# Optimization experiments

Measured on AMD Instinct MI355X. Metric: run time of the kernel, lower is better.

The kernel has to match this reference:

```python
import jax, jax.numpy as jnp
import numpy as np

EMBED_DIM = 128
NUM_EDGES = 4096   # edges per graph (power of 2)
BATCH = 64
N_LEAVES = BATCH * NUM_EDGES
NUM_LEVELS = int(np.log2(NUM_EDGES))  # 12


def setup_inputs() -> dict:
    key = jax.random.key(0)
    ks = jax.random.split(key, 4)
    d = EMBED_DIM
    scale = 1.0 / np.sqrt(2 * d)
    return {
        "h_bot": jax.random.normal(ks[0], (N_LEAVES, d), dtype=jnp.float32),
        "c_bot": jax.random.normal(ks[1], (N_LEAVES, d), dtype=jnp.float32),
        "U_iou": jax.random.normal(ks[2], (2 * d, 3 * d), dtype=jnp.float32) * scale,
        "b_iou": jnp.zeros((3 * d,), dtype=jnp.float32),
        "Uf_W": jax.random.normal(ks[3], (2 * d, 2 * d), dtype=jnp.float32) * scale,
        "Uf_b": jnp.zeros((2 * d,), dtype=jnp.float32),
    }


def _cell(hl, cl, hr, cr, U_iou, b_iou, Uf_W, Uf_b):
    # BinaryTreeLSTMCell: combine two child (h, c) states.
    h_cat = jnp.concatenate([hl, hr], axis=-1)          # [n, 2d]
    iou = h_cat @ U_iou + b_iou                          # [n, 3d]
    i, o, u = jnp.split(iou, 3, axis=-1)
    i = jax.nn.sigmoid(i)
    o = jax.nn.sigmoid(o)
    u = jnp.tanh(u)
    f = jax.nn.sigmoid(h_cat @ Uf_W + Uf_b)              # [n, 2d]
    f1, f2 = jnp.split(f, 2, axis=-1)
    c = i * u + f1 * cl + f2 * cr
    h = o * jnp.tanh(c)
    return h, c


def reference(h_bot, c_bot, U_iou, b_iou, Uf_W, Uf_b):
    # Per-level Fenwick merge: left children are states[0::2], right are
    # states[1::2] (as in get_list_indices), combined by the tree-LSTM cell.
    h, c = h_bot, c_bot
    for _ in range(NUM_LEVELS):
        h, c = _cell(h[0::2], c[0::2], h[1::2], c[1::2],
                     U_iou, b_iou, Uf_W, Uf_b)
    # one (h, c) root state per graph -> [BATCH, 2*EMBED_DIM]
    return jnp.concatenate([h, c], axis=-1)
```

## Files before the change

kernel.cpp:

```cpp
#include <hip/hip_runtime.h>
#include <hip/hip_bf16.h>
#include <stdint.h>


#define DEV __device__ __forceinline__

typedef __attribute__((ext_vector_type(8))) short bf16x8;
typedef __attribute__((ext_vector_type(4))) float f32x4;

DEV float bf2f(unsigned short u) {
    union { uint32_t i; float f; } v; v.i = ((uint32_t)u) << 16; return v.f;
}
DEV unsigned short f2bf(float f) {
    union { float f; uint32_t i; } v; v.f = f;
    uint32_t u = v.i;
    return (unsigned short)((u + 0x7FFFu + ((u >> 16) & 1u)) >> 16);
}
DEV unsigned short truncbf(float f) {
    union { float f; uint32_t i; } v; v.f = f; return (unsigned short)(v.i >> 16);
}
DEV float sigm(float x) { return 1.0f / (1.0f + __expf(-x)); }
DEV float tanh_(float x) {
    x = fminf(fmaxf(x, -15.f), 15.f);
    float e = __expf(2.0f * x);
    return (e - 1.0f) / (e + 1.0f);
}
DEV float ldmix(const void* p, size_t i, int bf) {
    return bf ? bf2f(((const unsigned short*)p)[i]) : ((const float*)p)[i];
}

__global__ void pack_w(const void* __restrict__ h_bot,
                       const void* __restrict__ U_iou, const void* __restrict__ Uf_W,
                       const void* __restrict__ b_iou, const void* __restrict__ uf_b,
                       int* __restrict__ flag_out, float* __restrict__ bias_out,
                       unsigned short* __restrict__ Wp) {
    __shared__ int total;
    const int tid = threadIdx.x;
    if (tid == 0) total = 0;
    __syncthreads();
    const unsigned short* hs = (const unsigned short*)h_bot;
    int local = 0;
    #pragma unroll
    for (int i = 0; i < 4; ++i) {
        unsigned short s = hs[tid * 4 + i];
        int e = (s >> 7) & 0xFF;
        local += (e >= 100 && e <= 134) ? 1 : 0;
    }
    atomicAdd(&total, local);
    __syncthreads();
    const int flag = (total > 820) ? 1 : 0;

    if (blockIdx.x == 0) {
        if (tid == 0) *flag_out = flag;
        for (int i = tid; i < 384; i += 256) bias_out[i]       = ldmix(b_iou, i, flag);
        for (int i = tid; i < 256; i += 256) bias_out[384 + i] = ldmix(uf_b, i, flag);
    }

    int idx  = blockIdx.x * 256 + tid;
    int j    = idx / 20480;
    int rem  = idx % 20480;
    int g    = rem / 4096;
    int rem2 = rem & 4095;
    int ks   = rem2 >> 9;
    int lane = (rem2 >> 3) & 63;
    int jj   = rem2 & 7;
    int k = ks * 32 + (lane >> 4) * 8 + jj;
    int t = j * 16 + (lane & 15);
    float w = (g < 3) ? ldmix(U_iou, (size_t)k * 384 + g * 128 + t, flag)
                      : ldmix(Uf_W,  (size_t)k * 256 + (g - 3) * 128 + t, flag);
    unsigned short hi = truncbf(w);
    unsigned short lo = f2bf(w - bf2f(hi));
    size_t base = (size_t)j * 40960;
    int fb = (g * 8 + ks) * 512 + lane * 8 + jj;
    Wp[base + fb]         = hi;
    Wp[base + 20480 + fb] = lo;
}

template<int IN_MODE, bool LEAN, bool FINAL, bool JSPLIT, int BLK, int MT>
__global__ __launch_bounds__(BLK, (BLK == 512 ? 4 : 2))
void level_kernel(const void* __restrict__ h_in,
                  const unsigned short* __restrict__ h_lo_in,
                  const void* __restrict__ c_in_v,
                  const unsigned short* __restrict__ Wp,
                  const int* __restrict__ flag_p,
                  const float* __restrict__ bias,
                  unsigned short* __restrict__ h_hi_out,
                  unsigned short* __restrict__ h_lo_out,
                  void* __restrict__ c_out_v,
                  void* __restrict__ final_out,
                  int M_out) {
    __shared__ __align__(16) unsigned short ldsW[40960];
    const int tid  = threadIdx.x;
    const int lane = tid & 63;
    const int w    = tid >> 6;
    const int ROWS = (BLK / 64) * MT * 16;
    const int R0   = blockIdx.x * ROWS + w * MT * 16;
    const int mrow = lane & 15;
    const int quad = lane >> 4;
    const int flag = (IN_MODE == 0 || FINAL) ? *flag_p : 0;

    const int    M_in   = 2 * M_out;
    const size_t PS_in  = (size_t)M_in  * 16;
    const size_t PS_out = (size_t)M_out * 16;

    bf16x8 a_hi[MT][8], a_lo[MT][8];
    #pragma unroll
    for (int mt = 0; mt < MT; ++mt) {
        int r = R0 + mt * 16 + mrow;
        if (r >= M_out) r = M_out - 1;
        #pragma unroll
        for (int ks = 0; ks < 8; ++ks) {
            if (IN_MODE == 0) {
                size_t base = ((size_t)(2 * r + (ks >> 2))) * 128 + (ks & 3) * 32 + quad * 8;
                if (flag) {
                    a_hi[mt][ks] = *(const bf16x8*)((const unsigned short*)h_in + base);
                    bf16x8 z;
                    #pragma unroll
                    for (int e = 0; e < 8; ++e) z[e] = 0;
                    a_lo[mt][ks] = z;
                } else {
                    const float* hf = (const float*)h_in;
                    f32x4 x0 = *(const f32x4*)(hf + base);
                    f32x4 x1 = *(const f32x4*)(hf + base + 4);
                    bf16x8 hv, lv;
                    #pragma unroll
                    for (int e = 0; e < 4; ++e) {
                        float x = x0[e];
                        unsigned short hh = truncbf(x);
                        hv[e] = (short)hh; lv[e] = (short)f2bf(x - bf2f(hh));
                    }
                    #pragma unroll
                    for (int e = 0; e < 4; ++e) {
                        float x = x1[e];
                        unsigned short hh = truncbf(x);
                        hv[4 + e] = (short)hh; lv[4 + e] = (short)f2bf(x - bf2f(hh));
                    }
                    a_hi[mt][ks] = hv; a_lo[mt][ks] = lv;
                }
            } else {
                int jpl = (ks & 3) * 2 + (quad >> 1);
                size_t base = (size_t)jpl * PS_in
                            + (size_t)(2 * r + (ks >> 2)) * 16 + (quad & 1) * 8;
                a_hi[mt][ks] = *(const bf16x8*)((const unsigned short*)h_in + base);
                if (IN_MODE == 1)
                    a_lo[mt][ks] = *(const bf16x8*)(h_lo_in + base);
            }
        }
    }

    const bf16x8* ldsV = (const bf16x8*)ldsW;
    const int jN = JSPLIT ? 1 : 8;

    #pragma unroll 1
    for (int jj = 0; jj < jN; ++jj) {
        const int j = JSPLIT ? (int)blockIdx.y : ((jj + (int)blockIdx.x) & 7);
        __syncthreads();
        {
            const bf16x8* src = (const bf16x8*)(Wp + (size_t)j * 40960);
            bf16x8*       dst = (bf16x8*)ldsW;
            #pragma unroll
            for (int it = tid; it < 5120; it += BLK)
                dst[it] = src[it];
        }
        __syncthreads();

        f32x4 acc[5][MT];
        #pragma unroll
        for (int g = 0; g < 5; ++g)
            #pragma unroll
            for (int mt = 0; mt < MT; ++mt)
                acc[g][mt] = f32x4{0.f, 0.f, 0.f, 0.f};
        #pragma unroll
        for (int ks = 0; ks < 8; ++ks) {
            #pragma unroll
            for (int g = 0; g < 5; ++g) {
                bf16x8 bhi = ldsV[(g * 8 + ks) * 64 + lane];
                bf16x8 blo = ldsV[(40 + g * 8 + ks) * 64 + lane];
                #pragma unroll
                for (int mt = 0; mt < MT; ++mt) {
                    acc[g][mt] = __builtin_amdgcn_mfma_f32_16x16x32_bf16(a_hi[mt][ks], bhi, acc[g][mt], 0, 0, 0);
                    if (IN_MODE != 2)
                        acc[g][mt] = __builtin_amdgcn_mfma_f32_16x16x32_bf16(a_lo[mt][ks], bhi, acc[g][mt], 0, 0, 0);
                    acc[g][mt] = __builtin_amdgcn_mfma_f32_16x16x32_bf16(a_hi[mt][ks], blo, acc[g][mt], 0, 0, 0);
                }
            }
        }

        const int t = j * 16 + mrow;
        const float bi   = bias[t];
        const float bo   = bias[128 + t];
        const float bu   = bias[256 + t];
        const float bf1v = bias[384 + t];
        const float bf2v = bias[512 + t];
        #pragma unroll
        for (int mt = 0; mt < MT; ++mt) {
            #pragma unroll
            for (int p = 0; p < 4; ++p) {
                int r = R0 + mt * 16 + quad * 4 + p;
                if (r < M_out) {
                    float iv = sigm(acc[0][mt][p] + bi);
                    float ov = sigm(acc[1][mt][p] + bo);
                    float uv = tanh_(acc[2][mt][p] + bu);
                    float f1 = sigm(acc[3][mt][p] + bf1v);
                    float f2 = sigm(acc[4][mt][p] + bf2v);
                    float cl, cr;
                    if (IN_MODE == 0) {
                        size_t li = ((size_t)(2 * r)) * 128 + t;
                        cl = ldmix(c_in_v, li, flag);
                        cr = ldmix(c_in_v, li + 128, flag);
                    } else {
                        size_t cb = (size_t)j * PS_in + (size_t)(2 * r) * 16 + mrow;
                        if (IN_MODE == 1) {
                            cl = ((const float*)c_in_v)[cb];
                            cr = ((const float*)c_in_v)[cb + 16];
                        } else {
                            cl = bf2f(((const unsigned short*)c_in_v)[cb]);
                            cr = bf2f(((const unsigned short*)c_in_v)[cb + 16]);
                        }
                    }
                    float c = fmaf(iv, uv, fmaf(f1, cl, f2 * cr));
                    float h = ov * tanh_(c);
                    if (FINAL) {
                        if (flag) {
                            unsigned short* o = (unsigned short*)final_out;
                            o[(size_t)r * 256 + t]       = f2bf(h);
                            o[(size_t)r * 256 + 128 + t] = f2bf(c);
                        } else {
                            float* o = (float*)final_out;
                            o[(size_t)r * 256 + t]       = h;
                            o[(size_t)r * 256 + 128 + t] = c;
                        }
                    } else {
                        size_t so = (size_t)j * PS_out + (size_t)r * 16 + mrow;
                        if (LEAN) {
                            h_hi_out[so] = f2bf(h);
                            ((unsigned short*)c_out_v)[so] = f2bf(c);
                        } else {
                            unsigned short hh = truncbf(h);
                            h_hi_out[so] = hh;
                            h_lo_out[so] = f2bf(h - bf2f(hh));
                            ((float*)c_out_v)[so] = c;
                        }
                    }
                }
            }
        }
    }
}

extern "C" void kernel_launch(void* const* d_in, const int* in_sizes, int n_in,
                              void* d_out, int out_size, void* d_ws, size_t ws_size,
                              hipStream_t stream) {
    const void* h_bot = d_in[0];
    const void* c_bot = d_in[1];
    const void* U_iou = d_in[2];
    const void* b_iou = d_in[3];
    const void* Uf_W  = d_in[4];
    const void* Uf_b  = d_in[5];
    (void)in_sizes; (void)n_in; (void)out_size;

    const int M0 = 131072;

    char* ws = (char*)d_ws;
    size_t off = 0;
    auto alloc = [&](size_t bytes) -> void* {
        off = (off + 255) & ~(size_t)255;
        void* p = ws + off;
        off += bytes;
        return p;
    };

    int*            flag = (int*)alloc(4);
    float*          bias = (float*)alloc(640 * 4);
    unsigned short* Wp   = (unsigned short*)alloc((size_t)327680 * 2);

    size_t full_need = off + 4096
                     + 2 * (size_t)33554432 + 2 * (size_t)16777216
                     + (size_t)67108864 + (size_t)33554432;
    bool full = (ws_size >= full_need);

    pack_w<<<dim3(640), dim3(256), 0, stream>>>(h_bot, U_iou, Uf_W, b_iou, Uf_b,
                                                flag, bias, Wp);

    if (full) {
        unsigned short* hAhi = (unsigned short*)alloc(33554432);
        unsigned short* hAlo = (unsigned short*)alloc(33554432);
        unsigned short* hBhi = (unsigned short*)alloc(16777216);
        unsigned short* hBlo = (unsigned short*)alloc(16777216);
        float*          cA   = (float*)alloc(67108864);
        float*          cB   = (float*)alloc(33554432);

        level_kernel<0, false, false, false, 512, 1><<<dim3(1024), dim3(512), 0, stream>>>(
            h_bot, nullptr, c_bot, Wp, flag, bias, hAhi, hAlo, cA, nullptr, M0);
        level_kernel<1, false, false, false, 512, 1><<<dim3(512), dim3(512), 0, stream>>>(
            hAhi, hAlo, cA, Wp, flag, bias, hBhi, hBlo, cB, nullptr, M0 >> 1);
        level_kernel<1, false, false, false, 512, 1><<<dim3(256), dim3(512), 0, stream>>>(
            hBhi, hBlo, cB, Wp, flag, bias, hAhi, hAlo, cA, nullptr, M0 >> 2);

        const unsigned short* hi_in = hAhi;
        const unsigned short* lo_in = hAlo;
        const void*           c_in  = cA;
        for (int l = 3; l < 11; ++l) {
            int M = M0 >> l;
            unsigned short* ohi = (l & 1) ? hBhi : hAhi;
            unsigned short* olo = (l & 1) ? hBlo : hAlo;
            float*          oc  = (l & 1) ? cB : cA;
            level_kernel<1, false, false, true, 256, 2>
                <<<dim3((M + 127) / 128, 8), dim3(256), 0, stream>>>(
                hi_in, lo_in, c_in, Wp, flag, bias, ohi, olo, oc, nullptr, M);
            hi_in = ohi; lo_in = olo; c_in = oc;
        }
        level_kernel<1, false, true, true, 256, 2><<<dim3(1, 8), dim3(256), 0, stream>>>(
            hi_in, lo_in, c_in, Wp, flag, bias, nullptr, nullptr, nullptr, d_out, 64);
    } else {
        unsigned short* hA = (unsigned short*)alloc(33554432);
        unsigned short* hB = (unsigned short*)alloc(16777216);
        unsigned short* cA = (unsigned short*)alloc(33554432);
        unsigned short* cB = (unsigned short*)alloc(16777216);

        level_kernel<0, true, false, false, 512, 1><<<dim3(1024), dim3(512), 0, stream>>>(
            h_bot, nullptr, c_bot, Wp, flag, bias, hA, nullptr, cA, nullptr, M0);
        level_kernel<2, true, false, false, 512, 1><<<dim3(512), dim3(512), 0, stream>>>(
            hA, nullptr, cA, Wp, flag, bias, hB, nullptr, cB, nullptr, M0 >> 1);
        level_kernel<2, true, false, false, 512, 1><<<dim3(256), dim3(512), 0, stream>>>(
            hB, nullptr, cB, Wp, flag, bias, hA, nullptr, cA, nullptr, M0 >> 2);

        const unsigned short* h_in = hA;
        const void*           c_in = cA;
        for (int l = 3; l < 11; ++l) {
            int M = M0 >> l;
            unsigned short* oh = (l & 1) ? hB : hA;
            unsigned short* oc = (l & 1) ? cB : cA;
            level_kernel<2, true, false, true, 256, 2>
                <<<dim3((M + 127) / 128, 8), dim3(256), 0, stream>>>(
                h_in, nullptr, c_in, Wp, flag, bias, oh, nullptr, oc, nullptr, M);
            h_in = oh; c_in = oc;
        }
        level_kernel<2, true, true, true, 256, 2><<<dim3(1, 8), dim3(256), 0, stream>>>(
            h_in, nullptr, c_in, Wp, flag, bias, nullptr, nullptr, nullptr, d_out, 64);
    }
}
```

Before: 700.4 us.

## Double-buffer weight staging via async global-to-LDS loads split into hi/lo phases

Splits each output-column tile's weights into two half-size phases (hi and lo terms) and double-buffers them in LDS, loading the next phase with global_load_lds while the current phase's MFMAs run. The c-state loads are moved ahead of the MFMA phase, and MFMA sections run at raised wave priority. This is meant to hide weight staging latency and the per-tile barrier stalls. The cost is more barriers per tile, extra registers for the prefetched c values, and a dependence on how the async LDS load is ordered against the barriers.

```diff
diff --git a/kernel.cpp b/kernel.cpp
--- a/kernel.cpp
+++ b/kernel.cpp
@@ -7,6 +7,9 @@
 
 typedef __attribute__((ext_vector_type(8))) short bf16x8;
 typedef __attribute__((ext_vector_type(4))) float f32x4;
+
+typedef __attribute__((address_space(3))) uint32_t lds_u32_t;
+typedef const __attribute__((address_space(1))) uint32_t glb_u32_t;
 
 DEV float bf2f(unsigned short u) {
     union { uint32_t i; float f; } v; v.i = ((uint32_t)u) << 16; return v.f;
@@ -27,6 +30,17 @@
 }
 DEV float ldmix(const void* p, size_t i, int bf) {
     return bf ? bf2f(((const unsigned short*)p)[i]) : ((const float*)p)[i];
+}
+
+template<int BLK>
+DEV void stage_term(unsigned short* dst, const unsigned short* src, int tid) {
+    constexpr int NIT = 40960 / (BLK * 16);
+    #pragma unroll
+    for (int it = 0; it < NIT; ++it) {
+        int o = (it * BLK + tid) * 8;
+        __builtin_amdgcn_global_load_lds((glb_u32_t*)(src + o),
+                                         (lds_u32_t*)(dst + o), 16, 0, 0);
+    }
 }
 
 __global__ void pack_w(const void* __restrict__ h_bot,
@@ -89,7 +103,7 @@
                   void* __restrict__ c_out_v,
                   void* __restrict__ final_out,
                   int M_out) {
-    __shared__ __align__(16) unsigned short ldsW[40960];
+    __shared__ __align__(16) unsigned short ldsW[2][20480];
     const int tid  = threadIdx.x;
     const int lane = tid & 63;
     const int w    = tid >> 6;
@@ -102,6 +116,15 @@
     const int    M_in   = 2 * M_out;
     const size_t PS_in  = (size_t)M_in  * 16;
     const size_t PS_out = (size_t)M_out * 16;
+
+    const int phN  = JSPLIT ? 2 : 16;
+    const int rot  = JSPLIT ? 0 : (int)blockIdx.x;
+    auto phSrc = [&](int ph) -> const unsigned short* {
+        int j = JSPLIT ? (int)blockIdx.y : ((ph >> 1) + rot) & 7;
+        return Wp + (size_t)j * 40960 + (size_t)(ph & 1) * 20480;
+    };
+
+    stage_term<BLK>(ldsW[0], phSrc(0), tid);
 
     bf16x8 a_hi[MT][8], a_lo[MT][8];
     #pragma unroll
@@ -148,64 +171,35 @@
         }
     }
 
-    const bf16x8* ldsV = (const bf16x8*)ldsW;
-    const int jN = JSPLIT ? 1 : 8;
-
+    __syncthreads();
+
+    f32x4 acc[5][MT];
+    #pragma unroll
+    for (int g = 0; g < 5; ++g)
+        #pragma unroll
+        for (int mt = 0; mt < MT; ++mt)
+            acc[g][mt] = f32x4{0.f, 0.f, 0.f, 0.f};
+    float cpre[MT][4][2];
+
+    int cur = 0;
     #pragma unroll 1
-    for (int jj = 0; jj < jN; ++jj) {
-        const int j = JSPLIT ? (int)blockIdx.y : ((jj + (int)blockIdx.x) & 7);
-        __syncthreads();
-        {
-            const bf16x8* src = (const bf16x8*)(Wp + (size_t)j * 40960);
-            bf16x8*       dst = (bf16x8*)ldsW;
+    for (int ph = 0; ph < phN; ++ph) {
+        const int j    = JSPLIT ? (int)blockIdx.y : ((ph >> 1) + rot) & 7;
+        const int term = ph & 1;
+
+        if (ph + 1 < phN)
+            stage_term<BLK>(ldsW[cur ^ 1], phSrc(ph + 1), tid);
+
+        if (term == 0) {
             #pragma unroll
-            for (int it = tid; it < 5120; it += BLK)
-                dst[it] = src[it];
-        }
-        __syncthreads();
-
-        f32x4 acc[5][MT];
-        #pragma unroll
-        for (int g = 0; g < 5; ++g)
-            #pragma unroll
-            for (int mt = 0; mt < MT; ++mt)
-                acc[g][mt] = f32x4{0.f, 0.f, 0.f, 0.f};
-        #pragma unroll
-        for (int ks = 0; ks < 8; ++ks) {
-            #pragma unroll
-            for (int g = 0; g < 5; ++g) {
-                bf16x8 bhi = ldsV[(g * 8 + ks) * 64 + lane];
-                bf16x8 blo = ldsV[(40 + g * 8 + ks) * 64 + lane];
+            for (int mt = 0; mt < MT; ++mt) {
                 #pragma unroll
-                for (int mt = 0; mt < MT; ++mt) {
-                    acc[g][mt] = __builtin_amdgcn_mfma_f32_16x16x32_bf16(a_hi[mt][ks], bhi, acc[g][mt], 0, 0, 0);
-                    if (IN_MODE != 2)
-                        acc[g][mt] = __builtin_amdgcn_mfma_f32_16x16x32_bf16(a_lo[mt][ks], bhi, acc[g][mt], 0, 0, 0);
-                    acc[g][mt] = __builtin_amdgcn_mfma_f32_16x16x32_bf16(a_hi[mt][ks], blo, acc[g][mt], 0, 0, 0);
-                }
-            }
-        }
-
-        const int t = j * 16 + mrow;
-        const float bi   = bias[t];
-        const float bo   = bias[128 + t];
-        const float bu   = bias[256 + t];
-        const float bf1v = bias[384 + t];
-        const float bf2v = bias[512 + t];
-        #pragma unroll
-        for (int mt = 0; mt < MT; ++mt) {
-            #pragma unroll
-            for (int p = 0; p < 4; ++p) {
-                int r = R0 + mt * 16 + quad * 4 + p;
-                if (r < M_out) {
-                    float iv = sigm(acc[0][mt][p] + bi);
-                    float ov = sigm(acc[1][mt][p] + bo);
-                    float uv = tanh_(acc[2][mt][p] + bu);
-                    float f1 = sigm(acc[3][mt][p] + bf1v);
-                    float f2 = sigm(acc[4][mt][p] + bf2v);
+                for (int p = 0; p < 4; ++p) {
+                    int r = R0 + mt * 16 + quad * 4 + p;
+                    if (r >= M_out) r = M_out - 1;
                     float cl, cr;
                     if (IN_MODE == 0) {
-                        size_t li = ((size_t)(2 * r)) * 128 + t;
+                        size_t li = ((size_t)(2 * r)) * 128 + j * 16 + mrow;
                         cl = ldmix(c_in_v, li, flag);
                         cr = ldmix(c_in_v, li + 128, flag);
                     } else {
@@ -218,33 +212,82 @@
                             cr = bf2f(((const unsigned short*)c_in_v)[cb + 16]);
                         }
                     }
-                    float c = fmaf(iv, uv, fmaf(f1, cl, f2 * cr));
-                    float h = ov * tanh_(c);
-                    if (FINAL) {
-                        if (flag) {
-                            unsigned short* o = (unsigned short*)final_out;
-                            o[(size_t)r * 256 + t]       = f2bf(h);
-                            o[(size_t)r * 256 + 128 + t] = f2bf(c);
+                    cpre[mt][p][0] = cl; cpre[mt][p][1] = cr;
+                }
+            }
+        }
+
+        const bf16x8* bufV = (const bf16x8*)ldsW[cur];
+        __builtin_amdgcn_s_setprio(1);
+        #pragma unroll
+        for (int ks = 0; ks < 8; ++ks) {
+            #pragma unroll
+            for (int g = 0; g < 5; ++g) {
+                bf16x8 b = bufV[(g * 8 + ks) * 64 + lane];
+                #pragma unroll
+                for (int mt = 0; mt < MT; ++mt) {
+                    acc[g][mt] = __builtin_amdgcn_mfma_f32_16x16x32_bf16(a_hi[mt][ks], b, acc[g][mt], 0, 0, 0);
+                    if (IN_MODE != 2 && term == 0)
+                        acc[g][mt] = __builtin_amdgcn_mfma_f32_16x16x32_bf16(a_lo[mt][ks], b, acc[g][mt], 0, 0, 0);
+                }
+            }
+        }
+        __builtin_amdgcn_s_setprio(0);
+
+        if (term == 1) {
+            const int t = j * 16 + mrow;
+            const float bi   = bias[t];
+            const float bo   = bias[128 + t];
+            const float bu   = bias[256 + t];
+            const float bf1v = bias[384 + t];
+            const float bf2v = bias[512 + t];
+            #pragma unroll
+            for (int mt = 0; mt < MT; ++mt) {
+                #pragma unroll
+                for (int p = 0; p < 4; ++p) {
+                    int r = R0 + mt * 16 + quad * 4 + p;
+                    if (r < M_out) {
+                        float iv = sigm(acc[0][mt][p] + bi);
+                        float ov = sigm(acc[1][mt][p] + bo);
+                        float uv = tanh_(acc[2][mt][p] + bu);
+                        float f1 = sigm(acc[3][mt][p] + bf1v);
+                        float f2 = sigm(acc[4][mt][p] + bf2v);
+                        float c = fmaf(iv, uv, fmaf(f1, cpre[mt][p][0], f2 * cpre[mt][p][1]));
+                        float h = ov * tanh_(c);
+                        if (FINAL) {
+                            if (flag) {
+                                unsigned short* o = (unsigned short*)final_out;
+                                o[(size_t)r * 256 + t]       = f2bf(h);
+                                o[(size_t)r * 256 + 128 + t] = f2bf(c);
+                            } else {
+                                float* o = (float*)final_out;
+                                o[(size_t)r * 256 + t]       = h;
+                                o[(size_t)r * 256 + 128 + t] = c;
+                            }
                         } else {
-                            float* o = (float*)final_out;
-                            o[(size_t)r * 256 + t]       = h;
-                            o[(size_t)r * 256 + 128 + t] = c;
-                        }
-                    } else {
-                        size_t so = (size_t)j * PS_out + (size_t)r * 16 + mrow;
-                        if (LEAN) {
-                            h_hi_out[so] = f2bf(h);
-                            ((unsigned short*)c_out_v)[so] = f2bf(c);
-                        } else {
-                            unsigned short hh = truncbf(h);
-                            h_hi_out[so] = hh;
-                            h_lo_out[so] = f2bf(h - bf2f(hh));
-                            ((float*)c_out_v)[so] = c;
+                            size_t so = (size_t)j * PS_out + (size_t)r * 16 + mrow;
+                            if (LEAN) {
+                                h_hi_out[so] = f2bf(h);
+                                ((unsigned short*)c_out_v)[so] = f2bf(c);
+                            } else {
+                                unsigned short hh = truncbf(h);
+                                h_hi_out[so] = hh;
+                                h_lo_out[so] = f2bf(h - bf2f(hh));
+                                ((float*)c_out_v)[so] = c;
+                            }
                         }
                     }
                 }
             }
-        }
+            #pragma unroll
+            for (int g = 0; g < 5; ++g)
+                #pragma unroll
+                for (int mt = 0; mt < MT; ++mt)
+                    acc[g][mt] = f32x4{0.f, 0.f, 0.f, 0.f};
+        }
+
+        if (ph + 1 < phN) __syncthreads();
+        cur ^= 1;
     }
 }
 
```

Result: no change. 706.3 us (+0.8%).
